# Kernel tuning notes

Hardware: AMD Instinct MI355X
Metric: run time of the kernel (lower is better)

## Reference

```python
import jax, jax.numpy as jnp
import numpy as np

B, S, D, H = 4, 1024, 1024, 16  # batch, seq_len, num_hiddens, num_heads
NEG = -1e6  # mask value used by the source's _sequence_mask


def setup_inputs() -> dict:
    key = jax.random.key(0)
    ks = jax.random.split(key, 8)
    f = lambda k, sh: (jax.random.normal(k, sh, dtype=jnp.float32) * 0.02)
    return {
        "queries": f(ks[0], (B, S, D)),
        "keys": f(ks[1], (B, S, D)),
        "values": f(ks[2], (B, S, D)),
        "valid_lens": jax.random.randint(ks[3], (B,), 1, S + 1),
        "Wq": f(ks[4], (D, D)),
        "Wk": f(ks[5], (D, D)),
        "Wv": f(ks[6], (D, D)),
        "Wo": f(ks[7], (D, D)),
    }


def reference(queries, keys, values, valid_lens, Wq, Wk, Wv, Wo):
    dh = D // H

    def split_heads(x):  # [B,S,D] -> [B,H,S,dh]
        return x.reshape(B, S, H, dh).transpose(0, 2, 1, 3)

    q = split_heads(queries @ Wq)
    k = split_heads(keys @ Wk)
    v = split_heads(values @ Wv)

    scores = jnp.einsum("bhqd,bhkd->bhqk", q, k) / jnp.sqrt(jnp.float32(dh))
    # per-batch key mask broadcast over heads and query positions: [B,1,1,S]
    mask = (jnp.arange(S)[None, :] < valid_lens[:, None])[:, None, None, :]
    scores = jnp.where(mask, scores, NEG)        # pre-softmax set to -1e6
    attn = jax.nn.softmax(scores, axis=-1)
    attn = jnp.where(mask, attn, 0.0)            # post-softmax zeroing (source quirk)
    out = jnp.einsum("bhqk,bhkd->bhqd", attn, v)  # [B,H,S,dh]
    # source uses permute(0,2,3,1): head-interleaved concat order
    concat = out.transpose(0, 2, 3, 1).reshape(B, S, D)
    return concat @ Wo
```

## Files before the change

kernel.cpp:

```cpp
#include <hip/hip_runtime.h>
#include <hip/hip_bf16.h>

#define BB 4
#define SS 1024
#define DDIM 1024
#define HH 16
#define MROWS (BB * SS)

typedef __attribute__((ext_vector_type(8))) short bf16x8;
typedef __attribute__((ext_vector_type(4))) float f32x4;

static __device__ __forceinline__ short f2bf(float x) {
    union { __hip_bfloat16 h; short s; } u;
    u.h = __float2bfloat16(x);
    return u.s;
}

#define GL_LDS16(gp, lp)                                                      \
    __builtin_amdgcn_global_load_lds(                                         \
        (const __attribute__((address_space(1))) void*)(gp),                  \
        (__attribute__((address_space(3))) void*)(lp), 16, 0, 0)

#define SWZ8(row, s) (((s) ^ ((row) & 7)) << 3)

static __device__ __forceinline__ void transposeW_body(const float* __restrict__ W,
                                                       short* __restrict__ dst,
                                                       int k0, int n0,
                                                       short (*sT)[72], int t) {
    {
        int r = t >> 2, cq = (t & 3) << 4;
        const float* p = W + (size_t)(k0 + r) * DDIM + n0 + cq;
        float4 a = ((const float4*)p)[0], b = ((const float4*)p)[1];
        float4 c = ((const float4*)p)[2], d = ((const float4*)p)[3];
        short* dp = &sT[r][cq];
        dp[0]  = f2bf(a.x); dp[1]  = f2bf(a.y); dp[2]  = f2bf(a.z); dp[3]  = f2bf(a.w);
        dp[4]  = f2bf(b.x); dp[5]  = f2bf(b.y); dp[6]  = f2bf(b.z); dp[7]  = f2bf(b.w);
        dp[8]  = f2bf(c.x); dp[9]  = f2bf(c.y); dp[10] = f2bf(c.z); dp[11] = f2bf(c.w);
        dp[12] = f2bf(d.x); dp[13] = f2bf(d.y); dp[14] = f2bf(d.z); dp[15] = f2bf(d.w);
    }
    __syncthreads();
    {
        int n = t >> 2, kq = (t & 3) << 4;
        bf16x8 o0, o1;
#pragma unroll
        for (int j = 0; j < 8; ++j) o0[j] = sT[kq + j][n];
#pragma unroll
        for (int j = 0; j < 8; ++j) o1[j] = sT[kq + 8 + j][n];
        short* q = dst + (size_t)(n0 + n) * DDIM + k0 + kq;
        *(bf16x8*)q = o0;
        *(bf16x8*)(q + 8) = o1;
    }
}

__global__ __launch_bounds__(256) void prep(const float* __restrict__ X0,
                                            const float* __restrict__ X1,
                                            const float* __restrict__ X2,
                                            const float* __restrict__ W0,
                                            const float* __restrict__ W1,
                                            const float* __restrict__ W2,
                                            short* __restrict__ dstA,
                                            short* __restrict__ Wt,
                                            const int* __restrict__ vlens) {
    __shared__ short sT[64][72];
    const int bx = blockIdx.x;
    const int t = threadIdx.x;
    if (bx < 768) {
        const int z = bx >> 8;
        const int rem = bx & 255;
        const float* W = (z == 0) ? W0 : (z == 1) ? W1 : W2;
        transposeW_body(W, Wt + (size_t)z * DDIM * DDIM,
                        (rem >> 4) * 64, (rem & 15) * 64, sT, t);
        return;
    }
    const int bc = bx - 768;
    const int z = bc >> 11;
    const int blk = bc & 2047;
    const int row0 = blk << 1;
    if (z >= 1) {
        const int bb = row0 >> 10;
        if ((row0 & 1023) >= vlens[bb]) return;
    }
    const float* X = (z == 0) ? X0 : (z == 1) ? X1 : X2;
    short* D = dstA + (size_t)z * MROWS * DDIM;
    const size_t base = (size_t)blk * 2048 + t * 8;
    const float4 x0 = ((const float4*)(X + base))[0];
    const float4 x1 = ((const float4*)(X + base))[1];
    bf16x8 vv;
    vv[0] = f2bf(x0.x); vv[1] = f2bf(x0.y); vv[2] = f2bf(x0.z); vv[3] = f2bf(x0.w);
    vv[4] = f2bf(x1.x); vv[5] = f2bf(x1.y); vv[6] = f2bf(x1.z); vv[7] = f2bf(x1.w);
    *(bf16x8*)(D + base) = vv;
}

__global__ __launch_bounds__(256) void transposeW3(const float* __restrict__ W0,
                                                   const float* __restrict__ W1,
                                                   const float* __restrict__ W2,
                                                   short* __restrict__ Wt) {
    __shared__ short sT[64][72];
    const int z = blockIdx.z;
    const float* W = (z == 0) ? W0 : (z == 1) ? W1 : W2;
    transposeW_body(W, Wt + (size_t)z * DDIM * DDIM,
                    blockIdx.y * 64, blockIdx.x * 64, sT, threadIdx.x);
}

__global__ __launch_bounds__(256) void transposeV(const short* __restrict__ v,
                                                  short* __restrict__ vT,
                                                  const int* __restrict__ vlens) {
    const int st = blockIdx.x, h = blockIdx.y, bb = blockIdx.z;
    if (st * 64 >= vlens[bb]) return;
    __shared__ short sT[64][72];
    const int t = threadIdx.x;
#pragma unroll
    for (int j = 0; j < 2; ++j) {
        int c = t + j * 256;
        int sr = c >> 3, co = (c & 7) << 3;
        *(bf16x8*)(&sT[sr][co]) =
            *(const bf16x8*)(v + (size_t)(bb * SS + st * 64 + sr) * DDIM + h * 64 + co);
    }
    __syncthreads();
    {
        int e = t >> 2, sq = (t & 3) << 4;
        bf16x8 o0, o1;
#pragma unroll
        for (int j = 0; j < 8; ++j) o0[j] = sT[sq + j][e];
#pragma unroll
        for (int j = 0; j < 8; ++j) o1[j] = sT[sq + 8 + j][e];
        short* dst = vT + ((size_t)(bb * HH + h) * 64 + e) * SS + st * 64 + sq;
        *(bf16x8*)dst = o0;
        *(bf16x8*)(dst + 8) = o1;
    }
}

template<bool A_F32, bool C_F32, int BN, bool SKIP, bool TRC>
__global__ __launch_bounds__(256) void gemm(const void* __restrict__ A0v,
                                            const void* __restrict__ A1v,
                                            const void* __restrict__ A2v,
                                            const short* __restrict__ BtBase,
                                            void* __restrict__ C0v,
                                            void* __restrict__ C1v,
                                            void* __restrict__ C2v,
                                            const int* __restrict__ vlens) {
    constexpr int NJ  = BN / 32;
    constexpr int NBX = DDIM / BN;
    constexpr int NPB = 32 * NBX;
    constexpr int BCH = BN / 32;

    __shared__ short smem[128 * 64 + BN * 64];
    short* sA = smem;
    short* sB = smem + 128 * 64;

    const int tid = threadIdx.x;
    const int lane = tid & 63, wid = tid >> 6;
    const int wr = wid >> 1, wc = wid & 1;
    const int g = lane >> 4, l15 = lane & 15;

    const int blk = blockIdx.x;
    const int z = blk / NPB;
    const int inner = blk % NPB;
    const int xcd = inner & 7, ii = inner >> 3;
    const int k4 = ii / NBX;
    const int by = k4 * 8 + ((xcd + 2 * k4) & 7);
    const int bx = ii % NBX;

    if constexpr (SKIP) {
        if (z >= 1 && ((by & 7) << 7) >= vlens[by >> 3]) return;
    }

    const void* Av = (z == 0) ? A0v : (z == 1) ? A1v : A2v;
    const short* Bt = BtBase + (size_t)z * DDIM * DDIM;
    void* Cv = (z == 0) ? C0v : (z == 1) ? C1v : C2v;
    const float* Af = (const float*)Av;
    const short* Ab = (const short*)Av;
    const int K = DDIM;

    f32x4 acc[4][NJ] = {};
    const int nkt = K >> 6;

    for (int t = 0; t < nkt; ++t) {
        const int kt = t << 6;
        __syncthreads();

        if constexpr (A_F32) {
            float4 ra[4][2];
#pragma unroll
            for (int j = 0; j < 4; ++j) {
                int c = tid + j * 256;
                int row = c >> 3, s = c & 7;
                const float* p = Af + (size_t)(by * 128 + row) * K + kt + s * 8;
                ra[j][0] = ((const float4*)p)[0];
                ra[j][1] = ((const float4*)p)[1];
            }
#pragma unroll
            for (int j = 0; j < 4; ++j) {
                int c = tid + j * 256;
                int row = c >> 3, s = c & 7;
                bf16x8 vv;
                vv[0] = f2bf(ra[j][0].x); vv[1] = f2bf(ra[j][0].y);
                vv[2] = f2bf(ra[j][0].z); vv[3] = f2bf(ra[j][0].w);
                vv[4] = f2bf(ra[j][1].x); vv[5] = f2bf(ra[j][1].y);
                vv[6] = f2bf(ra[j][1].z); vv[7] = f2bf(ra[j][1].w);
                *(bf16x8*)(&sA[row * 64 + SWZ8(row, s)]) = vv;
            }
        } else {
#pragma unroll
            for (int j = 0; j < 4; ++j) {
                int c = tid + j * 256;
                int row = c >> 3, sp = c & 7;
                GL_LDS16(Ab + (size_t)(by * 128 + row) * K + kt + SWZ8(row, sp),
                         (char*)sA + c * 16);
            }
        }
#pragma unroll
        for (int j = 0; j < BCH; ++j) {
            int c = tid + j * 256;
            int row = c >> 3, sp = c & 7;
            GL_LDS16(Bt + (size_t)(bx * BN + row) * K + kt + SWZ8(row, sp),
                     (char*)sB + c * 16);
        }
        __syncthreads();

        bf16x8 af[4][2], bfr[NJ][2];
#pragma unroll
        for (int i = 0; i < 4; ++i) {
            int row = wr * 64 + i * 16 + l15;
#pragma unroll
            for (int kh = 0; kh < 2; ++kh) {
                int s = kh * 4 + g;
                af[i][kh] = *(const bf16x8*)(&sA[row * 64 + SWZ8(row, s)]);
            }
        }
#pragma unroll
        for (int j = 0; j < NJ; ++j) {
            int row = wc * (BN / 2) + j * 16 + l15;
#pragma unroll
            for (int kh = 0; kh < 2; ++kh) {
                int s = kh * 4 + g;
                bfr[j][kh] = *(const bf16x8*)(&sB[row * 64 + SWZ8(row, s)]);
            }
        }
#pragma unroll
        for (int kh = 0; kh < 2; ++kh)
#pragma unroll
            for (int i = 0; i < 4; ++i)
#pragma unroll
                for (int j = 0; j < NJ; ++j)
                    acc[i][j] = __builtin_amdgcn_mfma_f32_16x16x32_bf16(af[i][kh], bfr[j][kh], acc[i][j], 0, 0, 0);
    }

    if constexpr (TRC && BN == 128) {
        if (z == 2) {
            __syncthreads();
            short* sT = smem;
#pragma unroll
            for (int i = 0; i < 4; ++i)
#pragma unroll
                for (int j = 0; j < NJ; ++j)
#pragma unroll
                    for (int r = 0; r < 4; ++r) {
                        int row = wr * 64 + i * 16 + g * 4 + r;
                        int col = wc * 64 + j * 16 + l15;
                        sT[col * 128 + ((((row >> 3) ^ (col & 7)) << 3) | (row & 7))] =
                            f2bf(acc[i][j][r]);
                    }
            __syncthreads();
            {
                int col = tid >> 1, half = tid & 1;
                int cg = bx * 128 + col;
                int h = cg >> 6, e = cg & 63;
                size_t R = ((size_t)(by >> 3) * HH + h) * 64 + e;
                short* dst = (short*)Cv + R * SS + (size_t)(by & 7) * 128 + half * 64;
#pragma unroll
                for (int m = 0; m < 8; ++m) {
                    int mm = half * 8 + m;
                    bf16x8 ch = *(const bf16x8*)(&sT[col * 128 + ((mm ^ (col & 7)) << 3)]);
                    *(bf16x8*)(dst + m * 8) = ch;
                }
            }
            return;
        }
    }

#pragma unroll
    for (int i = 0; i < 4; ++i)
#pragma unroll
        for (int j = 0; j < NJ; ++j)
#pragma unroll
            for (int r = 0; r < 4; ++r) {
                int row = by * 128 + wr * 64 + i * 16 + g * 4 + r;
                int col = bx * BN + wc * (BN / 2) + j * 16 + l15;
                if constexpr (C_F32)
                    ((float*)Cv)[(size_t)row * DDIM + col] = acc[i][j][r];
                else
                    ((short*)Cv)[(size_t)row * DDIM + col] = f2bf(acc[i][j][r]);
            }
}

template<bool TRV, bool WOT>
__global__ __launch_bounds__(256) void attn(const short* __restrict__ q,
                                            const short* __restrict__ k,
                                            const short* __restrict__ v,
                                            const int* __restrict__ vlens,
                                            short* __restrict__ att,
                                            const float* __restrict__ Wo,
                                            short* __restrict__ wt_o) {
    __shared__ short asmem[20480];
    const int tid = threadIdx.x;
    int blk = blockIdx.x;
    if constexpr (WOT) {
        if (blk < 256) {
            transposeW_body(Wo, wt_o, (blk >> 4) * 64, (blk & 15) * 64,
                            (short (*)[72])asmem, tid);
            return;
        }
        blk -= 256;
    }

    const int qt = blk >> 6;
    const int hb = blk & 63;
    const int bb = hb & 3;
    const int h  = hb >> 2;

    const int lane = tid & 63, wid = tid >> 6;
    const int g = lane >> 4, l15 = lane & 15;
    const int vlen = vlens[bb];
    const int pOff = 16384 + wid * 1024;

    const int srow = qt * 64 + wid * 16 + l15;
    const short* qrow = q + ((size_t)(bb * SS + srow)) * DDIM + h * 64;
    bf16x8 qf[2];
    qf[0] = *(const bf16x8*)(qrow + g * 8);
    qf[1] = *(const bf16x8*)(qrow + 32 + g * 8);

    float lsum[4] = {0.f, 0.f, 0.f, 0.f};
    f32x4 oacc[4] = {};

    const int key0 = tid >> 3, key1 = (tid + 256) >> 3, sp = tid & 7;
    const int d0 = (tid & 7) << 3;
    const short* vTb = v + ((size_t)(bb * HH + h) * 64) * SS;

    const int ntiles = (vlen + 63) >> 6;

    {
        GL_LDS16(k + ((size_t)(bb * SS + key0)) * DDIM + h * 64 + ((sp ^ (key0 & 7)) << 3),
                 (char*)&asmem[0] + tid * 16);
        GL_LDS16(k + ((size_t)(bb * SS + key1)) * DDIM + h * 64 + ((sp ^ (key1 & 7)) << 3),
                 (char*)&asmem[0] + (tid + 256) * 16);
        if constexpr (TRV) {
            GL_LDS16(vTb + (size_t)key0 * SS + ((sp ^ (key0 & 7)) << 3),
                     (char*)&asmem[8192] + tid * 16);
            GL_LDS16(vTb + (size_t)key1 * SS + ((sp ^ (key1 & 7)) << 3),
                     (char*)&asmem[8192] + (tid + 256) * 16);
        } else {
            bf16x8 v0 = *(const bf16x8*)(v + ((size_t)(bb * SS + key0)) * DDIM + h * 64 + d0);
            bf16x8 v1 = *(const bf16x8*)(v + ((size_t)(bb * SS + key1)) * DDIM + h * 64 + d0);
#pragma unroll
            for (int e = 0; e < 8; ++e) {
                int e0 = d0 + e;
                asmem[8192 + e0 * 64 + (((key0 >> 3) ^ (e0 & 7)) << 3) + (key0 & 7)] = v0[e];
                asmem[8192 + e0 * 64 + (((key1 >> 3) ^ (e0 & 7)) << 3) + (key1 & 7)] = v1[e];
            }
        }
    }
    __syncthreads();

    for (int t = 0; t < ntiles; ++t) {
        const int cur = t & 1, nxt = cur ^ 1;
        const int kOffC = cur * 4096, kOffN = nxt * 4096;
        const int vOffC = 8192 + cur * 4096, vOffN = 8192 + nxt * 4096;
        const int kb = t * 64;
        const bool pre = (t + 1 < ntiles);

        bf16x8 vr0, vr1;
        if (pre) {
            const int kb2 = kb + 64;
            GL_LDS16(k + ((size_t)(bb * SS + kb2 + key0)) * DDIM + h * 64 + ((sp ^ (key0 & 7)) << 3),
                     (char*)&asmem[0] + kOffN * 2 + tid * 16);
            GL_LDS16(k + ((size_t)(bb * SS + kb2 + key1)) * DDIM + h * 64 + ((sp ^ (key1 & 7)) << 3),
                     (char*)&asmem[0] + kOffN * 2 + (tid + 256) * 16);
            if constexpr (TRV) {
                GL_LDS16(vTb + (size_t)key0 * SS + kb2 + ((sp ^ (key0 & 7)) << 3),
                         (char*)&asmem[0] + vOffN * 2 + tid * 16);
                GL_LDS16(vTb + (size_t)key1 * SS + kb2 + ((sp ^ (key1 & 7)) << 3),
                         (char*)&asmem[0] + vOffN * 2 + (tid + 256) * 16);
            } else {
                vr0 = *(const bf16x8*)(v + ((size_t)(bb * SS + kb2 + key0)) * DDIM + h * 64 + d0);
                vr1 = *(const bf16x8*)(v + ((size_t)(bb * SS + kb2 + key1)) * DDIM + h * 64 + d0);
            }
        }

        f32x4 sacc[4] = {};
#pragma unroll
        for (int kg = 0; kg < 4; ++kg) {
            int row = kg * 16 + l15;
#pragma unroll
            for (int kh = 0; kh < 2; ++kh) {
                int s = kh * 4 + g;
                bf16x8 kf = *(const bf16x8*)(&asmem[kOffC + row * 64 + ((s ^ (row & 7)) << 3)]);
                sacc[kg] = __builtin_amdgcn_mfma_f32_16x16x32_bf16(qf[kh], kf, sacc[kg], 0, 0, 0);
            }
        }

#pragma unroll
        for (int r = 0; r < 4; ++r) {
            float p[4], ls = 0.f;
#pragma unroll
            for (int kg = 0; kg < 4; ++kg) {
                float s = fminf(sacc[kg][r] * 0.125f, 60.0f);
                if (kb + kg * 16 + l15 >= vlen) s = -1e30f;
                p[kg] = __expf(s);
                ls += p[kg];
            }
            lsum[r] += ls;
            const int srw = g * 4 + r;
#pragma unroll
            for (int kg = 0; kg < 4; ++kg) {
                int col = kg * 16 + l15;
                asmem[pOff + srw * 64 + (((col >> 3) ^ (srw & 7)) << 3) + (col & 7)] = f2bf(p[kg]);
            }
        }

        bf16x8 pf[2];
#pragma unroll
        for (int kh = 0; kh < 2; ++kh) {
            int s = kh * 4 + g;
            pf[kh] = *(const bf16x8*)(&asmem[pOff + l15 * 64 + ((s ^ (l15 & 7)) << 3)]);
        }
#pragma unroll
        for (int n = 0; n < 4; ++n) {
            const int e = n * 16 + l15;
#pragma unroll
            for (int kh = 0; kh < 2; ++kh) {
                int s = kh * 4 + g;
                bf16x8 vf = *(const bf16x8*)(&asmem[vOffC + e * 64 + ((s ^ (e & 7)) << 3)]);
                oacc[n] = __builtin_amdgcn_mfma_f32_16x16x32_bf16(pf[kh], vf, oacc[n], 0, 0, 0);
            }
        }

        if constexpr (!TRV) {
            if (pre) {
#pragma unroll
                for (int e = 0; e < 8; ++e) {
                    int e0 = d0 + e;
                    asmem[vOffN + e0 * 64 + (((key0 >> 3) ^ (e0 & 7)) << 3) + (key0 & 7)] = vr0[e];
                    asmem[vOffN + e0 * 64 + (((key1 >> 3) ^ (e0 & 7)) << 3) + (key1 & 7)] = vr1[e];
                }
            }
        }
        __syncthreads();
    }

#pragma unroll
    for (int r = 0; r < 4; ++r) {
        float rs = lsum[r];
#pragma unroll
        for (int off = 1; off < 16; off <<= 1)
            rs += __shfl_xor(rs, off);
        lsum[r] = rs;
    }

#pragma unroll
    for (int n = 0; n < 4; ++n)
#pragma unroll
        for (int r = 0; r < 4; ++r) {
            float o = oacc[n][r] / lsum[r];
            int sg = qt * 64 + wid * 16 + g * 4 + r;
            int e = n * 16 + l15;
            att[((size_t)(bb * SS + sg)) * DDIM + e * HH + h] = f2bf(o);
        }
}

extern "C" void kernel_launch(void* const* d_in, const int* in_sizes, int n_in,
                              void* d_out, int out_size, void* d_ws, size_t ws_size,
                              hipStream_t stream) {
    const float* queries = (const float*)d_in[0];
    const float* keys    = (const float*)d_in[1];
    const float* values  = (const float*)d_in[2];
    const int*   vlens   = (const int*)d_in[3];
    const float* Wq      = (const float*)d_in[4];
    const float* Wk      = (const float*)d_in[5];
    const float* Wv      = (const float*)d_in[6];
    const float* Wo      = (const float*)d_in[7];
    float* out = (float*)d_out;

    short* ws = (short*)d_ws;
    const size_t sz = (size_t)MROWS * DDIM;
    short* q_ws   = ws;
    short* k_ws   = ws + sz;
    short* reg2   = ws + 2 * sz;
    short* att_ws = ws + 3 * sz;
    short* wt3    = att_ws;

    const size_t regionB = sz * sizeof(short);
    const bool big = ws_size >= 7 * regionB;
    const bool mid = ws_size >= 5 * regionB;

    if (big) {
        short* qb = ws + 4 * sz;
        short* kb = ws + 5 * sz;
        short* vb = ws + 6 * sz;
        prep<<<dim3(6912), 256, 0, stream>>>(queries, keys, values,
                                             Wq, Wk, Wv, qb, wt3, vlens);
        gemm<false, false, 128, true, true><<<dim3(768), 256, 0, stream>>>(
            qb, kb, vb, wt3, q_ws, k_ws, reg2, vlens);
        attn<true, true><<<dim3(1280), 256, 0, stream>>>(
            q_ws, k_ws, reg2, vlens, att_ws, Wo, vb);
        gemm<false, true, 64, false, false><<<dim3(512), 256, 0, stream>>>(
            att_ws, att_ws, att_ws, vb, out, out, out, vlens);
    } else if (mid) {
        short* vT = ws + 4 * sz;
        short* wt_o = q_ws;
        transposeW3<<<dim3(16, 16, 3), 256, 0, stream>>>(Wq, Wk, Wv, wt3);
        gemm<true, false, 128, true, false><<<dim3(768), 256, 0, stream>>>(
            queries, keys, values, wt3, q_ws, k_ws, reg2, vlens);
        transposeV<<<dim3(16, 16, 4), 256, 0, stream>>>(reg2, vT, vlens);
        attn<true, false><<<dim3(1024), 256, 0, stream>>>(
            q_ws, k_ws, vT, vlens, att_ws, Wo, wt_o);
        transposeW3<<<dim3(16, 16, 1), 256, 0, stream>>>(Wo, Wo, Wo, wt_o);
        gemm<false, true, 64, false, false><<<dim3(512), 256, 0, stream>>>(
            att_ws, att_ws, att_ws, wt_o, out, out, out, vlens);
    } else {
        short* wt_o = q_ws;
        transposeW3<<<dim3(16, 16, 3), 256, 0, stream>>>(Wq, Wk, Wv, wt3);
        gemm<true, false, 128, true, false><<<dim3(768), 256, 0, stream>>>(
            queries, keys, values, wt3, q_ws, k_ws, reg2, vlens);
        attn<false, false><<<dim3(1024), 256, 0, stream>>>(
            q_ws, k_ws, reg2, vlens, att_ws, Wo, wt_o);
        transposeW3<<<dim3(16, 16, 1), 256, 0, stream>>>(Wo, Wo, Wo, wt_o);
        gemm<false, true, 64, false, false><<<dim3(512), 256, 0, stream>>>(
            att_ws, att_ws, att_ws, wt_o, out, out, out, vlens);
    }
}
```

Measured before the change: 89.21 us.

## Process two 64-row query tiles per attention block to reuse K/V tiles

Each attention block now holds query fragments and accumulators for 128 query rows (two 64-row sub-tiles) instead of 64. Every K/V tile loaded into shared memory is used twice, which halves global-to-LDS traffic and barrier count per query row. The attention grid is halved to match. In exchange, register pressure roughly doubles for accumulators, there are fewer blocks to hide latency, and load balance across CUs gets coarser, especially with variable valid lengths.

```diff
diff --git a/kernel.cpp b/kernel.cpp
--- a/kernel.cpp
+++ b/kernel.cpp
@@ -324,14 +324,17 @@
     const int vlen = vlens[bb];
     const int pOff = 16384 + wid * 1024;
 
-    const int srow = qt * 64 + wid * 16 + l15;
-    const short* qrow = q + ((size_t)(bb * SS + srow)) * DDIM + h * 64;
-    bf16x8 qf[2];
-    qf[0] = *(const bf16x8*)(qrow + g * 8);
-    qf[1] = *(const bf16x8*)(qrow + 32 + g * 8);
-
-    float lsum[4] = {0.f, 0.f, 0.f, 0.f};
-    f32x4 oacc[4] = {};
+    bf16x8 qf[2][2];
+#pragma unroll
+    for (int qs = 0; qs < 2; ++qs) {
+        const int srow = qt * 128 + qs * 64 + wid * 16 + l15;
+        const short* qrow = q + ((size_t)(bb * SS + srow)) * DDIM + h * 64;
+        qf[qs][0] = *(const bf16x8*)(qrow + g * 8);
+        qf[qs][1] = *(const bf16x8*)(qrow + 32 + g * 8);
+    }
+
+    float lsum[2][4] = {};
+    f32x4 oacc[2][4] = {};
 
     const int key0 = tid >> 3, key1 = (tid + 256) >> 3, sp = tid & 7;
     const int d0 = (tid & 7) << 3;
@@ -387,51 +390,54 @@
             }
         }
 
-        f32x4 sacc[4] = {};
-#pragma unroll
-        for (int kg = 0; kg < 4; ++kg) {
-            int row = kg * 16 + l15;
+#pragma unroll
+        for (int qs = 0; qs < 2; ++qs) {
+            f32x4 sacc[4] = {};
+#pragma unroll
+            for (int kg = 0; kg < 4; ++kg) {
+                int row = kg * 16 + l15;
+#pragma unroll
+                for (int kh = 0; kh < 2; ++kh) {
+                    int s = kh * 4 + g;
+                    bf16x8 kf = *(const bf16x8*)(&asmem[kOffC + row * 64 + ((s ^ (row & 7)) << 3)]);
+                    sacc[kg] = __builtin_amdgcn_mfma_f32_16x16x32_bf16(qf[qs][kh], kf, sacc[kg], 0, 0, 0);
+                }
+            }
+
+#pragma unroll
+            for (int r = 0; r < 4; ++r) {
+                float p[4], ls = 0.f;
+#pragma unroll
+                for (int kg = 0; kg < 4; ++kg) {
+                    float s = fminf(sacc[kg][r] * 0.125f, 60.0f);
+                    if (kb + kg * 16 + l15 >= vlen) s = -1e30f;
+                    p[kg] = __expf(s);
+                    ls += p[kg];
+                }
+                lsum[qs][r] += ls;
+                const int srw = g * 4 + r;
+#pragma unroll
+                for (int kg = 0; kg < 4; ++kg) {
+                    int col = kg * 16 + l15;
+                    asmem[pOff + srw * 64 + (((col >> 3) ^ (srw & 7)) << 3) + (col & 7)] = f2bf(p[kg]);
+                }
+            }
+
+            bf16x8 pf[2];
 #pragma unroll
             for (int kh = 0; kh < 2; ++kh) {
                 int s = kh * 4 + g;
-                bf16x8 kf = *(const bf16x8*)(&asmem[kOffC + row * 64 + ((s ^ (row & 7)) << 3)]);
-                sacc[kg] = __builtin_amdgcn_mfma_f32_16x16x32_bf16(qf[kh], kf, sacc[kg], 0, 0, 0);
-            }
-        }
-
-#pragma unroll
-        for (int r = 0; r < 4; ++r) {
-            float p[4], ls = 0.f;
-#pragma unroll
-            for (int kg = 0; kg < 4; ++kg) {
-                float s = fminf(sacc[kg][r] * 0.125f, 60.0f);
-                if (kb + kg * 16 + l15 >= vlen) s = -1e30f;
-                p[kg] = __expf(s);
-                ls += p[kg];
-            }
-            lsum[r] += ls;
-            const int srw = g * 4 + r;
-#pragma unroll
-            for (int kg = 0; kg < 4; ++kg) {
-                int col = kg * 16 + l15;
-                asmem[pOff + srw * 64 + (((col >> 3) ^ (srw & 7)) << 3) + (col & 7)] = f2bf(p[kg]);
-            }
-        }
-
-        bf16x8 pf[2];
-#pragma unroll
-        for (int kh = 0; kh < 2; ++kh) {
-            int s = kh * 4 + g;
-            pf[kh] = *(const bf16x8*)(&asmem[pOff + l15 * 64 + ((s ^ (l15 & 7)) << 3)]);
-        }
-#pragma unroll
-        for (int n = 0; n < 4; ++n) {
-            const int e = n * 16 + l15;
-#pragma unroll
-            for (int kh = 0; kh < 2; ++kh) {
-                int s = kh * 4 + g;
-                bf16x8 vf = *(const bf16x8*)(&asmem[vOffC + e * 64 + ((s ^ (e & 7)) << 3)]);
-                oacc[n] = __builtin_amdgcn_mfma_f32_16x16x32_bf16(pf[kh], vf, oacc[n], 0, 0, 0);
+                pf[kh] = *(const bf16x8*)(&asmem[pOff + l15 * 64 + ((s ^ (l15 & 7)) << 3)]);
+            }
+#pragma unroll
+            for (int n = 0; n < 4; ++n) {
+                const int e = n * 16 + l15;
+#pragma unroll
+                for (int kh = 0; kh < 2; ++kh) {
+                    int s = kh * 4 + g;
+                    bf16x8 vf = *(const bf16x8*)(&asmem[vOffC + e * 64 + ((s ^ (e & 7)) << 3)]);
+                    oacc[qs][n] = __builtin_amdgcn_mfma_f32_16x16x32_bf16(pf[kh], vf, oacc[qs][n], 0, 0, 0);
+                }
             }
         }
 
@@ -449,23 +455,25 @@
     }
 
 #pragma unroll
-    for (int r = 0; r < 4; ++r) {
-        float rs = lsum[r];
-#pragma unroll
-        for (int off = 1; off < 16; off <<= 1)
-            rs += __shfl_xor(rs, off);
-        lsum[r] = rs;
-    }
-
-#pragma unroll
-    for (int n = 0; n < 4; ++n)
+    for (int qs = 0; qs < 2; ++qs) {
 #pragma unroll
         for (int r = 0; r < 4; ++r) {
-            float o = oacc[n][r] / lsum[r];
-            int sg = qt * 64 + wid * 16 + g * 4 + r;
-            int e = n * 16 + l15;
-            att[((size_t)(bb * SS + sg)) * DDIM + e * HH + h] = f2bf(o);
-        }
+            float rs = lsum[qs][r];
+#pragma unroll
+            for (int off = 1; off < 16; off <<= 1)
+                rs += __shfl_xor(rs, off);
+            lsum[qs][r] = rs;
+        }
+#pragma unroll
+        for (int n = 0; n < 4; ++n)
+#pragma unroll
+            for (int r = 0; r < 4; ++r) {
+                float o = oacc[qs][n][r] / lsum[qs][r];
+                int sg = qt * 128 + qs * 64 + wid * 16 + g * 4 + r;
+                int e = n * 16 + l15;
+                att[((size_t)(bb * SS + sg)) * DDIM + e * HH + h] = f2bf(o);
+            }
+    }
 }
 
 extern "C" void kernel_launch(void* const* d_in, const int* in_sizes, int n_in,
@@ -501,7 +509,7 @@
                                              Wq, Wk, Wv, qb, wt3, vlens);
         gemm<false, false, 128, true, true><<<dim3(768), 256, 0, stream>>>(
             qb, kb, vb, wt3, q_ws, k_ws, reg2, vlens);
-        attn<true, true><<<dim3(1280), 256, 0, stream>>>(
+        attn<true, true><<<dim3(768), 256, 0, stream>>>(
             q_ws, k_ws, reg2, vlens, att_ws, Wo, vb);
         gemm<false, true, 64, false, false><<<dim3(512), 256, 0, stream>>>(
             att_ws, att_ws, att_ws, vb, out, out, out, vlens);
@@ -512,7 +520,7 @@
         gemm<true, false, 128, true, false><<<dim3(768), 256, 0, stream>>>(
             queries, keys, values, wt3, q_ws, k_ws, reg2, vlens);
         transposeV<<<dim3(16, 16, 4), 256, 0, stream>>>(reg2, vT, vlens);
-        attn<true, false><<<dim3(1024), 256, 0, stream>>>(
+        attn<true, false><<<dim3(512), 256, 0, stream>>>(
             q_ws, k_ws, vT, vlens, att_ws, Wo, wt_o);
         transposeW3<<<dim3(16, 16, 1), 256, 0, stream>>>(Wo, Wo, Wo, wt_o);
         gemm<false, true, 64, false, false><<<dim3(512), 256, 0, stream>>>(
@@ -522,7 +530,7 @@
         transposeW3<<<dim3(16, 16, 3), 256, 0, stream>>>(Wq, Wk, Wv, wt3);
         gemm<true, false, 128, true, false><<<dim3(768), 256, 0, stream>>>(
             queries, keys, values, wt3, q_ws, k_ws, reg2, vlens);
-        attn<false, false><<<dim3(1024), 256, 0, stream>>>(
+        attn<false, false><<<dim3(512), 256, 0, stream>>>(
             q_ws, k_ws, reg2, vlens, att_ws, Wo, wt_o);
         transposeW3<<<dim3(16, 16, 1), 256, 0, stream>>>(Wo, Wo, Wo, wt_o);
         gemm<false, true, 64, false, false><<<dim3(512), 256, 0, stream>>>(
```

Measured after the change: 91.57 us. 2.6% more time.
